# Kernel tuning notes

Hardware: AMD Instinct MI355X
Metric: run time of the kernel (lower is better)

The kernel has to match this reference:

```python
import jax, jax.numpy as jnp
import numpy as np

RES = (32, 32, 32)   # S, H, W
WS = 4               # window size (cubic)
SHIFT = 2            # shift size
NH = 6               # num heads
C = 192              # dim
EPS = 1e-5


def _rel_pos_index(ws):
    coords = np.stack(np.meshgrid(np.arange(ws), np.arange(ws), np.arange(ws), indexing='ij'))
    cf = coords.reshape(3, -1)                      # (3, N)
    rc = (cf[:, :, None] - cf[:, None, :]).transpose(1, 2, 0).astype(np.int64)  # (N,N,3)
    rc[..., 0] += ws - 1
    rc[..., 1] += ws - 1
    rc[..., 2] += ws - 1
    rc[..., 0] *= 3 * ws - 1
    rc[..., 1] *= 2 * ws - 1
    return rc.sum(-1)                               # (N, N)

_RPI = jnp.asarray(_rel_pos_index(WS))


def _ln(x, g, b):
    m = jnp.mean(x, axis=-1, keepdims=True)
    v = jnp.mean(jnp.square(x - m), axis=-1, keepdims=True)
    return (x - m) * jax.lax.rsqrt(v + EPS) * g + b


def setup_inputs():
    key = jax.random.key(0)
    ks = jax.random.split(key, 12)
    B, L = 2, RES[0] * RES[1] * RES[2]
    nW, N = 512, WS ** 3
    Hd = 4 * C
    p = lambda k, s: jax.random.normal(k, s, jnp.float32) * 0.02
    return {
        'x': jax.random.normal(ks[0], (B, L, C), jnp.float32),
        'mask_matrix': jax.random.normal(ks[1], (nW, N, N), jnp.float32),
        'skip': jax.random.normal(ks[2], (B, L, C), jnp.float32),
        'x_up': jax.random.normal(ks[3], (B, L, C), jnp.float32),
        'norm1_g': jnp.ones((C,), jnp.float32), 'norm1_b': jnp.zeros((C,), jnp.float32),
        'kv_w': p(ks[4], (C, 2 * C)), 'kv_b': jnp.zeros((2 * C,), jnp.float32),
        'rpb_table': p(ks[5], ((2 * WS - 1) ** 3, NH)),
        'proj_w': p(ks[6], (C, C)), 'proj_b': jnp.zeros((C,), jnp.float32),
        'norm2_g': jnp.ones((C,), jnp.float32), 'norm2_b': jnp.zeros((C,), jnp.float32),
        'fc1_w': p(ks[7], (C, Hd)), 'fc1_b': jnp.zeros((Hd,), jnp.float32),
        'fc2_w': p(ks[8], (Hd, C)), 'fc2_b': jnp.zeros((C,), jnp.float32),
    }


def reference(x, mask_matrix, skip, x_up, norm1_g, norm1_b, kv_w, kv_b, rpb_table,
              proj_w, proj_b, norm2_g, norm2_b, fc1_w, fc1_b, fc2_w, fc2_b):
    B, L, _ = x.shape
    S, H, W = RES
    ws, N = WS, WS ** 3
    hd = C // NH
    scale = hd ** -0.5

    sn = _ln(skip, norm1_g, norm1_b).reshape(B, S, H, W, C)
    qn = _ln(x_up, norm1_g, norm1_b).reshape(B, S, H, W, C)
    # cyclic shift (shift_size > 0)
    sn = jnp.roll(sn, (-SHIFT, -SHIFT, -SHIFT), axis=(1, 2, 3))
    qn = jnp.roll(qn, (-SHIFT, -SHIFT, -SHIFT), axis=(1, 2, 3))

    def part(t):  # window partition -> (B*nW, N, C)
        t = t.reshape(B, S // ws, ws, H // ws, ws, W // ws, ws, C)
        return t.transpose(0, 1, 3, 5, 2, 4, 6, 7).reshape(-1, N, C)

    skw, qw = part(sn), part(qn)
    B_ = skw.shape[0]

    kv = (skw @ kv_w + kv_b).reshape(B_, N, 2, NH, hd)
    k = kv[:, :, 0].transpose(0, 2, 1, 3)   # (B_, NH, N, hd)
    v = kv[:, :, 1].transpose(0, 2, 1, 3)
    q = qw.reshape(B_, N, NH, hd).transpose(0, 2, 1, 3) * scale

    attn = jnp.einsum('bhqd,bhkd->bhqk', q, k)
    rpb = rpb_table[_RPI.reshape(-1)].reshape(N, N, NH).transpose(2, 0, 1)  # (NH, N, N)
    attn = attn + rpb[None]
    nW = mask_matrix.shape[0]
    attn = attn.reshape(B, nW, NH, N, N) + mask_matrix[None, :, None]
    attn = jax.nn.softmax(attn.reshape(B_, NH, N, N), axis=-1)

    out = jnp.einsum('bhqk,bhkd->bhqd', attn, v).transpose(0, 2, 1, 3).reshape(B_, N, C)
    out = out @ proj_w + proj_b

    # window reverse
    out = out.reshape(B, S // ws, H // ws, W // ws, ws, ws, ws, C)
    out = out.transpose(0, 1, 4, 2, 5, 3, 6, 7).reshape(B, S, H, W, C)
    out = jnp.roll(out, (SHIFT, SHIFT, SHIFT), axis=(1, 2, 3)).reshape(B, L, C)

    x = x + out
    h = _ln(x, norm2_g, norm2_b)
    h = jax.nn.gelu(h @ fc1_w + fc1_b, approximate=False) @ fc2_w + fc2_b
    return x + h
```

## Files before the change

kernel.cpp:

```cpp
#include <hip/hip_runtime.h>
#include <math.h>

typedef unsigned short u16;
typedef __bf16 bf16x8 __attribute__((ext_vector_type(8)));
typedef float f32x4 __attribute__((ext_vector_type(4)));
typedef unsigned short u16x8 __attribute__((ext_vector_type(8)));

#define SHIFT 2

static __device__ __forceinline__ f32x4 mfma16(bf16x8 a, bf16x8 b, f32x4 c) {
  return __builtin_amdgcn_mfma_f32_16x16x32_bf16(a, b, c, 0, 0, 0);
}
static __device__ __forceinline__ u16 f2bf(float f) {
  unsigned u = __builtin_bit_cast(unsigned, f);
  unsigned r = u + 0x7fffu + ((u >> 16) & 1u);
  return (u16)(r >> 16);
}
static __device__ __forceinline__ float bf2f(u16 u) {
  unsigned v = (unsigned)u << 16;
  return __builtin_bit_cast(float, v);
}
static __device__ __forceinline__ void stage16(const u16* g, u16* lbase, int lane) {
#if __has_builtin(__builtin_amdgcn_global_load_lds)
  __builtin_amdgcn_global_load_lds(
      (const __attribute__((address_space(1))) unsigned int*)g,
      (__attribute__((address_space(3))) unsigned int*)lbase, 16, 0, 0);
#else
  *(u16x8*)(lbase + lane * 8) = *(const u16x8*)g;
#endif
}

#define OFF_KVWT  ((size_t)0)
#define OFF_PRWT  (OFF_KVWT + 384*192*2)
#define OFF_FC1WT (OFF_PRWT + 192*192*2)
#define OFF_FC2WT (OFF_FC1WT + 768*192*2)
#define OFF_SKW   (OFF_FC2WT + 192*768*2)
#define OFF_QW    (OFF_SKW + (size_t)65536*192*2)
#define OFF_KVB   (OFF_QW + (size_t)65536*192*2)
#define OFF_HN    (OFF_KVB + (size_t)65536*384*2)
#define OFF_PO    (OFF_HN + (size_t)65536*192*2)

__global__ __launch_bounds__(256) void k_prep(
    const float* __restrict__ kv_w, const float* __restrict__ proj_w,
    const float* __restrict__ fc1_w, const float* __restrict__ fc2_w,
    u16* __restrict__ kvT, u16* __restrict__ prT,
    u16* __restrict__ f1T, u16* __restrict__ f2T) {
  int i = blockIdx.x * 256 + threadIdx.x;
  if (i < 192 * 384) kvT[(i % 384) * 192 + i / 384] = f2bf(kv_w[i]);
  if (i < 192 * 192) prT[(i % 192) * 192 + i / 192] = f2bf(proj_w[i]);
  if (i < 192 * 768) f1T[(i % 768) * 192 + i / 768] = f2bf(fc1_w[i]);
  if (i < 768 * 192) f2T[(i % 192) * 768 + i / 192] = f2bf(fc2_w[i]);
}

__global__ __launch_bounds__(256) void k_ln_part(
    const float* __restrict__ skip, const float* __restrict__ x_up,
    const float* __restrict__ gam, const float* __restrict__ bet,
    u16* __restrict__ skw, u16* __restrict__ qw) {
  int row = blockIdx.x * 4 + (threadIdx.x >> 6);
  int lane = threadIdx.x & 63;
  const float* sp = skip + (size_t)row * 192;
  const float* qp = x_up + (size_t)row * 192;
  float sv[3], qv[3], ss = 0.f, qs = 0.f;
#pragma unroll
  for (int j = 0; j < 3; j++) {
    sv[j] = sp[lane + 64 * j]; qv[j] = qp[lane + 64 * j];
    ss += sv[j]; qs += qv[j];
  }
#pragma unroll
  for (int m = 1; m < 64; m <<= 1) { ss += __shfl_xor(ss, m, 64); qs += __shfl_xor(qs, m, 64); }
  float sm = ss * (1.f / 192.f), qm = qs * (1.f / 192.f);
  float s2 = 0.f, q2 = 0.f;
#pragma unroll
  for (int j = 0; j < 3; j++) { float d = sv[j] - sm; s2 += d * d; d = qv[j] - qm; q2 += d * d; }
#pragma unroll
  for (int m = 1; m < 64; m <<= 1) { s2 += __shfl_xor(s2, m, 64); q2 += __shfl_xor(q2, m, 64); }
  float sr = rsqrtf(s2 * (1.f / 192.f) + 1e-5f), qr = rsqrtf(q2 * (1.f / 192.f) + 1e-5f);
  int b = row >> 15, l = row & 32767;
  int s = l >> 10, h = (l >> 5) & 31, w = l & 31;
  int s_ = (s - SHIFT) & 31, h_ = (h - SHIFT) & 31, w_ = (w - SHIFT) & 31;
  int wIdx = ((s_ >> 2) * 8 + (h_ >> 2)) * 8 + (w_ >> 2);
  int n = ((s_ & 3) * 4 + (h_ & 3)) * 4 + (w_ & 3);
  size_t orow = ((size_t)(b * 512 + wIdx) * 64 + n) * 192;
  const float scale = 0.17677669529663687f;
#pragma unroll
  for (int j = 0; j < 3; j++) {
    int cc = lane + 64 * j;
    float gg = gam[cc], bb = bet[cc];
    skw[orow + cc] = f2bf((sv[j] - sm) * sr * gg + bb);
    qw[orow + cc]  = f2bf(((qv[j] - qm) * qr * gg + bb) * scale);
  }
}

__global__ __launch_bounds__(256, 2) void k_kv(
    const u16* __restrict__ A, const u16* __restrict__ BT,
    const float* __restrict__ bias, u16* __restrict__ outh) {
  __shared__ u16 lw[192 * 192];
  int mb = blockIdx.x, nb = blockIdx.y;
  int tid = threadIdx.x, l = tid & 63, wv = tid >> 6, g = l >> 4, c = l & 15;
  int wr = wv >> 1, wc = wv & 1;
#pragma unroll
  for (int i = 0; i < 18; i++) {
    int CI = i * 256 + tid;
    int row = CI / 24, ch = CI % 24;
    int sch = (ch & 24) | ((ch ^ row) & 7);
    stage16(BT + (size_t)(nb * 192 + row) * 192 + sch * 8, lw + (i * 256 + wv * 64) * 8, l);
  }
  __syncthreads();
  f32x4 acc[4][6] = {};
#pragma unroll
  for (int ks = 0; ks < 6; ks++) {
    bf16x8 a[4];
#pragma unroll
    for (int m = 0; m < 4; m++)
      a[m] = *(const bf16x8*)&A[(size_t)(mb * 128 + wr * 64 + m * 16 + c) * 192 + ks * 32 + g * 8];
#pragma unroll
    for (int n = 0; n < 6; n++) {
      int col = wc * 96 + n * 16 + c;
      int ch = ks * 4 + g;
      int chp = (ch & 24) | ((ch ^ col) & 7);
      bf16x8 b = *(const bf16x8*)&lw[col * 192 + chp * 8];
#pragma unroll
      for (int m = 0; m < 4; m++) acc[m][n] = mfma16(a[m], b, acc[m][n]);
    }
  }
#pragma unroll
  for (int n = 0; n < 6; n++)
#pragma unroll
    for (int m = 0; m < 4; m++) {
      int col = nb * 192 + wc * 96 + n * 16 + c;
      float bb = bias[col];
#pragma unroll
      for (int r = 0; r < 4; r++) {
        int row = mb * 128 + wr * 64 + m * 16 + g * 4 + r;
        outh[(size_t)row * 384 + col] = f2bf(acc[m][n][r] + bb);
      }
    }
}

__global__ __launch_bounds__(384, 4) void k_attn_mega(
    const u16* __restrict__ qw, const u16* __restrict__ kvb,
    const float* __restrict__ rpb, const float* __restrict__ mask,
    const u16* __restrict__ prT, const float* __restrict__ proj_b,
    const float* __restrict__ x, const float* __restrict__ g2,
    const float* __restrict__ b2, u16* __restrict__ hn, u16* __restrict__ po) {
  __shared__ __align__(16) char smem[25600 + 13824 + 17408 + 8256];
  u16* lv = (u16*)smem;
  u16* lo = (u16*)smem;
  u16* lp = (u16*)(smem + 25600);
  float* pf = (float*)(smem + 25600);
  float* lmaskf = (float*)(smem + 25600 + 13824);
  float* lrpbf  = (float*)(smem + 25600 + 13824 + 17408);
  int b_ = blockIdx.x, wIdx = b_ & 511;
  int tid = threadIdx.x, l = tid & 63, wv = tid >> 6, g = l >> 4, c = l & 15;
  int h = wv;
#pragma unroll
  for (int i = 0; i < 4; i++) {
    int CI = i * 384 + tid;
    int row = CI / 24, ch = CI % 24;
    stage16(kvb + ((size_t)b_ * 64 + row) * 384 + 192 + ch * 8,
            lv + (i * 384 + wv * 64) * 8, l);
  }
  bf16x8 qa[4], kb[4];
#pragma unroll
  for (int m = 0; m < 4; m++)
    qa[m] = *(const bf16x8*)&qw[((size_t)b_ * 64 + m * 16 + c) * 192 + h * 32 + g * 8];
#pragma unroll
  for (int n = 0; n < 4; n++)
    kb[n] = *(const bf16x8*)&kvb[((size_t)b_ * 64 + n * 16 + c) * 384 + h * 32 + g * 8];
  const float* mrow = mask + (size_t)wIdx * 4096;
#pragma unroll
  for (int i = 0; i < 3; i++) {
    int idx = i * 384 + tid;
    if (idx < 1024) {
      float4 mv = *(const float4*)&mrow[idx * 4];
      int row = idx >> 4, c4 = idx & 15;
      *(float4*)&lmaskf[row * 68 + c4 * 4] = mv;
    }
  }
#pragma unroll
  for (int i = 0; i < 6; i++) {
    int idx = i * 384 + tid;
    if (idx < 2058) lrpbf[idx] = rpb[idx];
  }
  __syncthreads();
  bf16x8 vb[2][2];
#pragma unroll
  for (int kk = 0; kk < 2; kk++)
#pragma unroll
    for (int nd = 0; nd < 2; nd++) {
      union { u16 u[8]; bf16x8 v; } bb;
#pragma unroll
      for (int j = 0; j < 8; j++)
        bb.u[j] = lv[(kk * 32 + g * 8 + j) * 192 + h * 32 + nd * 16 + c];
      vb[kk][nd] = bb.v;
    }
  __syncthreads();
  f32x4 acc[4][4] = {};
#pragma unroll
  for (int m = 0; m < 4; m++)
#pragma unroll
    for (int n = 0; n < 4; n++) acc[m][n] = mfma16(qa[m], kb[n], acc[m][n]);
  f32x4 oacc[4][2] = {};
#pragma unroll
  for (int m = 0; m < 4; m++) {
#pragma unroll
    for (int r = 0; r < 4; r++) {
      int qr = m * 16 + g * 4 + r;
      int qs = qr >> 4, qh = (qr >> 2) & 3, qx = qr & 3;
      float vals[4];
#pragma unroll
      for (int n = 0; n < 4; n++) {
        int kc = n * 16 + c;
        int ks = kc >> 4, kh = (kc >> 2) & 3, kx = kc & 3;
        int idx = (qs - ks + 3) * 11 + (qh - kh + 3) * 7 + (qx - kx + 3);
        vals[n] = acc[m][n][r] + lrpbf[idx * 6 + h] + lmaskf[qr * 68 + kc];
      }
      float mx = fmaxf(fmaxf(vals[0], vals[1]), fmaxf(vals[2], vals[3]));
#pragma unroll
      for (int mm = 1; mm < 16; mm <<= 1) mx = fmaxf(mx, __shfl_xor(mx, mm, 64));
      float sum = 0.f;
#pragma unroll
      for (int n = 0; n < 4; n++) { vals[n] = __expf(vals[n] - mx); sum += vals[n]; }
#pragma unroll
      for (int mm = 1; mm < 16; mm <<= 1) sum += __shfl_xor(sum, mm, 64);
      float inv = 1.f / sum;
#pragma unroll
      for (int n = 0; n < 4; n++)
        lp[h * 1152 + (g * 4 + r) * 72 + n * 16 + c] = f2bf(vals[n] * inv);
    }
#pragma unroll
    for (int kk = 0; kk < 2; kk++) {
      bf16x8 pa = *(const bf16x8*)&lp[h * 1152 + c * 72 + kk * 32 + g * 8];
#pragma unroll
      for (int nd = 0; nd < 2; nd++) oacc[m][nd] = mfma16(pa, vb[kk][nd], oacc[m][nd]);
    }
  }
#pragma unroll
  for (int m = 0; m < 4; m++)
#pragma unroll
    for (int nd = 0; nd < 2; nd++)
#pragma unroll
      for (int r = 0; r < 4; r++)
        lo[(m * 16 + g * 4 + r) * 200 + h * 32 + nd * 16 + c] = f2bf(oacc[m][nd][r]);
  __syncthreads();
  f32x4 pacc[4][2] = {};
#pragma unroll
  for (int ks = 0; ks < 6; ks++) {
    bf16x8 pa[4];
#pragma unroll
    for (int m = 0; m < 4; m++)
      pa[m] = *(const bf16x8*)&lo[(m * 16 + c) * 200 + ks * 32 + g * 8];
#pragma unroll
    for (int n = 0; n < 2; n++) {
      bf16x8 pb = *(const bf16x8*)&prT[(size_t)(wv * 32 + n * 16 + c) * 192 + ks * 32 + g * 8];
#pragma unroll
      for (int m = 0; m < 4; m++) pacc[m][n] = mfma16(pa[m], pb, pacc[m][n]);
    }
  }
  int bI = b_ >> 9;
  int wS = wIdx >> 6, wH = (wIdx >> 3) & 7, wW = wIdx & 7;
  float yv[4][2][4];
#pragma unroll
  for (int m = 0; m < 4; m++)
#pragma unroll
    for (int r = 0; r < 4; r++) {
      int tok = m * 16 + g * 4 + r;
      int inS = tok >> 4, inH = (tok >> 2) & 3, inW = tok & 3;
      int s = (wS * 4 + inS + SHIFT) & 31;
      int hh = (wH * 4 + inH + SHIFT) & 31;
      int ww = (wW * 4 + inW + SHIFT) & 31;
      size_t base = ((size_t)bI * 32768 + ((size_t)s * 32 + hh) * 32 + ww) * 192;
      float sum = 0.f, sq = 0.f;
#pragma unroll
      for (int n = 0; n < 2; n++) {
        int col = wv * 32 + n * 16 + c;
        float v = pacc[m][n][r] + proj_b[col];
        po[base + col] = f2bf(v);
        float y = v + x[base + col];
        yv[m][n][r] = y;
        sum += y; sq += y * y;
      }
#pragma unroll
      for (int mm = 1; mm < 16; mm <<= 1) { sum += __shfl_xor(sum, mm, 64); sq += __shfl_xor(sq, mm, 64); }
      if (c == 0) { pf[tok * 16 + wv] = sum; pf[tok * 16 + 8 + wv] = sq; }
    }
  __syncthreads();
#pragma unroll
  for (int m = 0; m < 4; m++)
#pragma unroll
    for (int r = 0; r < 4; r++) {
      int tok = m * 16 + g * 4 + r;
      int inS = tok >> 4, inH = (tok >> 2) & 3, inW = tok & 3;
      int s = (wS * 4 + inS + SHIFT) & 31;
      int hh = (wH * 4 + inH + SHIFT) & 31;
      int ww = (wW * 4 + inW + SHIFT) & 31;
      size_t base = ((size_t)bI * 32768 + ((size_t)s * 32 + hh) * 32 + ww) * 192;
      float su = 0.f, qu = 0.f;
#pragma unroll
      for (int w6 = 0; w6 < 6; w6++) { su += pf[tok * 16 + w6]; qu += pf[tok * 16 + 8 + w6]; }
      float mu = su * (1.f / 192.f);
      float rs = rsqrtf(qu * (1.f / 192.f) - mu * mu + 1e-5f);
#pragma unroll
      for (int n = 0; n < 2; n++) {
        int col = wv * 32 + n * 16 + c;
        hn[base + col] = f2bf((yv[m][n][r] - mu) * rs * g2[col] + b2[col]);
      }
    }
}

__global__ __launch_bounds__(256, 2) void k_mlp(
    const u16* __restrict__ hn, const u16* __restrict__ f1T,
    const u16* __restrict__ f2T, const float* __restrict__ b1,
    const float* __restrict__ b2f, const float* __restrict__ x,
    const u16* __restrict__ po, float* __restrict__ out) {
  __shared__ u16 lds[29184];
  u16* f1c = lds;
  u16* f2c = lds + 12288;
  u16* h1c = lds + 24576;
  int tid = threadIdx.x, l = tid & 63, wv = tid >> 6, g = l >> 4, c = l & 15;
  size_t tokbase = (size_t)blockIdx.x * 64;
#pragma unroll
  for (int i = 0; i < 6; i++) {
    int CI = i * 256 + wv * 64 + l;
    int row = CI / 24, chp = CI % 24;
    int sch = (chp & 24) | ((chp ^ row) & 7);
    stage16(hn + (tokbase + row) * 192 + sch * 8, f1c + (i * 256 + wv * 64) * 8, l);
  }
  __syncthreads();
  bf16x8 hb[4][6];
#pragma unroll
  for (int tf = 0; tf < 4; tf++)
#pragma unroll
    for (int ks = 0; ks < 6; ks++) {
      int ch = ks * 4 + g;
      int chp = (ch & 24) | ((ch ^ c) & 7);
      hb[tf][ks] = *(const bf16x8*)&f1c[(tf * 16 + c) * 192 + chp * 8];
    }
  f32x4 acc2[3][4] = {};
#pragma unroll 1
  for (int ko = 0; ko < 12; ko++) {
    __syncthreads();
#pragma unroll
    for (int i = 0; i < 6; i++) {
      int CI = i * 256 + wv * 64 + l;
      int row = CI / 24, chp = CI % 24;
      int sch = (chp & 24) | ((chp ^ row) & 7);
      stage16(f1T + (size_t)(ko * 64 + row) * 192 + sch * 8,
              f1c + (i * 256 + wv * 64) * 8, l);
    }
#pragma unroll
    for (int i = 0; i < 6; i++) {
      int CI = i * 256 + wv * 64 + l;
      int row = CI >> 3, chp = CI & 7;
      int sch = chp ^ (row & 7);
      stage16(f2T + (size_t)row * 768 + ko * 64 + sch * 8,
              f2c + (i * 256 + wv * 64) * 8, l);
    }
    __syncthreads();
    f32x4 acc1[4] = {};
#pragma unroll
    for (int ks = 0; ks < 6; ks++) {
      int ch = ks * 4 + g;
      int chp = (ch & 24) | ((ch ^ c) & 7);
      bf16x8 wa = *(const bf16x8*)&f1c[(wv * 16 + c) * 192 + chp * 8];
#pragma unroll
      for (int tf = 0; tf < 4; tf++) acc1[tf] = mfma16(wa, hb[tf][ks], acc1[tf]);
    }
    float4 b1v = *(const float4*)&b1[ko * 64 + wv * 16 + g * 4];
#pragma unroll
    for (int tf = 0; tf < 4; tf++) {
      unsigned pk[2];
#pragma unroll
      for (int p = 0; p < 2; p++) {
        unsigned lohi[2];
#pragma unroll
        for (int q = 0; q < 2; q++) {
          int r = p * 2 + q;
          float v = acc1[tf][r] + (r == 0 ? b1v.x : r == 1 ? b1v.y : r == 2 ? b1v.z : b1v.w);
          float u2 = v * (1.5957691216f + 0.0713548163f * v * v);
          v = v * (1.f / (1.f + __expf(-u2)));
          lohi[q] = f2bf(v);
        }
        pk[p] = lohi[0] | (lohi[1] << 16);
      }
      *(uint2*)&h1c[(tf * 16 + c) * 72 + wv * 16 + g * 4] = make_uint2(pk[0], pk[1]);
    }
    __syncthreads();
#pragma unroll
    for (int ck = 0; ck < 2; ck++) {
      bf16x8 a2[4];
#pragma unroll
      for (int tf = 0; tf < 4; tf++)
        a2[tf] = *(const bf16x8*)&h1c[(tf * 16 + c) * 72 + ck * 32 + g * 8];
#pragma unroll
      for (int of = 0; of < 3; of++) {
        int ch = ck * 4 + g;
        int chp = ch ^ (c & 7);
        bf16x8 wb = *(const bf16x8*)&f2c[(wv * 48 + of * 16 + c) * 64 + chp * 8];
#pragma unroll
        for (int tf = 0; tf < 4; tf++) acc2[of][tf] = mfma16(a2[tf], wb, acc2[of][tf]);
      }
    }
  }
#pragma unroll
  for (int of = 0; of < 3; of++)
#pragma unroll
    for (int tf = 0; tf < 4; tf++) {
      int col = wv * 48 + of * 16 + c;
      float bb = b2f[col];
#pragma unroll
      for (int r = 0; r < 4; r++) {
        size_t tok = tokbase + tf * 16 + g * 4 + r;
        size_t base = tok * 192 + col;
        out[base] = acc2[of][tf][r] + bb + x[base] + bf2f(po[base]);
      }
    }
}

extern "C" void kernel_launch(void* const* d_in, const int* in_sizes, int n_in,
                              void* d_out, int out_size, void* d_ws, size_t ws_size,
                              hipStream_t stream) {
  const float* x      = (const float*)d_in[0];
  const float* mask   = (const float*)d_in[1];
  const float* skip   = (const float*)d_in[2];
  const float* x_up   = (const float*)d_in[3];
  const float* n1g    = (const float*)d_in[4];
  const float* n1b    = (const float*)d_in[5];
  const float* kv_w   = (const float*)d_in[6];
  const float* kv_b   = (const float*)d_in[7];
  const float* rpb    = (const float*)d_in[8];
  const float* proj_w = (const float*)d_in[9];
  const float* proj_b = (const float*)d_in[10];
  const float* n2g    = (const float*)d_in[11];
  const float* n2b    = (const float*)d_in[12];
  const float* fc1_w  = (const float*)d_in[13];
  const float* fc1_b  = (const float*)d_in[14];
  const float* fc2_w  = (const float*)d_in[15];
  const float* fc2_b  = (const float*)d_in[16];
  char* ws = (char*)d_ws;
  u16* kvT  = (u16*)(ws + OFF_KVWT);
  u16* prT  = (u16*)(ws + OFF_PRWT);
  u16* f1T  = (u16*)(ws + OFF_FC1WT);
  u16* f2T  = (u16*)(ws + OFF_FC2WT);
  u16* skw  = (u16*)(ws + OFF_SKW);
  u16* qw   = (u16*)(ws + OFF_QW);
  u16* kvb  = (u16*)(ws + OFF_KVB);
  u16* hn   = (u16*)(ws + OFF_HN);
  u16* po   = (u16*)(ws + OFF_PO);
  float* out = (float*)d_out;

  k_prep<<<dim3(576), dim3(256), 0, stream>>>(kv_w, proj_w, fc1_w, fc2_w, kvT, prT, f1T, f2T);
  k_ln_part<<<dim3(16384), dim3(256), 0, stream>>>(skip, x_up, n1g, n1b, skw, qw);
  k_kv<<<dim3(512, 2), dim3(256), 0, stream>>>(skw, kvT, kv_b, kvb);
  k_attn_mega<<<dim3(1024), dim3(384), 0, stream>>>(
      qw, kvb, rpb, mask, prT, proj_b, x, n2g, n2b, hn, po);
  k_mlp<<<dim3(1024), dim3(256), 0, stream>>>(hn, f1T, f2T, fc1_b, fc2_b, x, po, out);
}
```

Before: 260.8 us.

## Precompute expanded bf16 relative-position bias and read mask directly from global

The relative position bias is expanded once per call in the prep kernel into a per-head 64x64 bf16 table, and the mask is no longer staged in LDS; both are read directly from global memory inside the softmax loop. This cuts the attention kernel's shared memory from about 65 KB to 38 KB and raises the launch-bounds occupancy hint from 4 to 6 blocks. It adds a sync before the output LDS reuse, since the P buffer now overlaps the output staging area. The costs are strided, uncoalesced global loads for mask and bias in the hot loop, and the bias rounded to bf16.

```diff
diff --git a/kernel.cpp b/kernel.cpp
--- a/kernel.cpp
+++ b/kernel.cpp
@@ -39,17 +39,26 @@
 #define OFF_KVB   (OFF_QW + (size_t)65536*192*2)
 #define OFF_HN    (OFF_KVB + (size_t)65536*384*2)
 #define OFF_PO    (OFF_HN + (size_t)65536*192*2)
+#define OFF_RPBG  (OFF_PO + (size_t)65536*192*2)
 
 __global__ __launch_bounds__(256) void k_prep(
     const float* __restrict__ kv_w, const float* __restrict__ proj_w,
     const float* __restrict__ fc1_w, const float* __restrict__ fc2_w,
+    const float* __restrict__ rpb,
     u16* __restrict__ kvT, u16* __restrict__ prT,
-    u16* __restrict__ f1T, u16* __restrict__ f2T) {
+    u16* __restrict__ f1T, u16* __restrict__ f2T, u16* __restrict__ rpbg) {
   int i = blockIdx.x * 256 + threadIdx.x;
   if (i < 192 * 384) kvT[(i % 384) * 192 + i / 384] = f2bf(kv_w[i]);
   if (i < 192 * 192) prT[(i % 192) * 192 + i / 192] = f2bf(proj_w[i]);
   if (i < 192 * 768) f1T[(i % 768) * 192 + i / 768] = f2bf(fc1_w[i]);
   if (i < 768 * 192) f2T[(i % 192) * 768 + i / 192] = f2bf(fc2_w[i]);
+  if (i < 24576) {
+    int h = i >> 12, rem = i & 4095, qr = rem >> 6, kc = rem & 63;
+    int qs = qr >> 4, qh = (qr >> 2) & 3, qx = qr & 3;
+    int ks = kc >> 4, kh = (kc >> 2) & 3, kx = kc & 3;
+    int idx = (qs - ks + 3) * 11 + (qh - kh + 3) * 7 + (qx - kx + 3);
+    rpbg[i] = f2bf(rpb[idx * 6 + h]);
+  }
 }
 
 __global__ __launch_bounds__(256) void k_ln_part(
@@ -137,19 +146,17 @@
     }
 }
 
-__global__ __launch_bounds__(384, 4) void k_attn_mega(
+__global__ __launch_bounds__(384, 6) void k_attn_mega(
     const u16* __restrict__ qw, const u16* __restrict__ kvb,
-    const float* __restrict__ rpb, const float* __restrict__ mask,
+    const u16* __restrict__ rpbg, const float* __restrict__ mask,
     const u16* __restrict__ prT, const float* __restrict__ proj_b,
     const float* __restrict__ x, const float* __restrict__ g2,
     const float* __restrict__ b2, u16* __restrict__ hn, u16* __restrict__ po) {
-  __shared__ __align__(16) char smem[25600 + 13824 + 17408 + 8256];
+  __shared__ __align__(16) char smem[38400];
   u16* lv = (u16*)smem;
   u16* lo = (u16*)smem;
-  u16* lp = (u16*)(smem + 25600);
+  u16* lp = (u16*)(smem + 24576);
   float* pf = (float*)(smem + 25600);
-  float* lmaskf = (float*)(smem + 25600 + 13824);
-  float* lrpbf  = (float*)(smem + 25600 + 13824 + 17408);
   int b_ = blockIdx.x, wIdx = b_ & 511;
   int tid = threadIdx.x, l = tid & 63, wv = tid >> 6, g = l >> 4, c = l & 15;
   int h = wv;
@@ -167,21 +174,6 @@
 #pragma unroll
   for (int n = 0; n < 4; n++)
     kb[n] = *(const bf16x8*)&kvb[((size_t)b_ * 64 + n * 16 + c) * 384 + h * 32 + g * 8];
-  const float* mrow = mask + (size_t)wIdx * 4096;
-#pragma unroll
-  for (int i = 0; i < 3; i++) {
-    int idx = i * 384 + tid;
-    if (idx < 1024) {
-      float4 mv = *(const float4*)&mrow[idx * 4];
-      int row = idx >> 4, c4 = idx & 15;
-      *(float4*)&lmaskf[row * 68 + c4 * 4] = mv;
-    }
-  }
-#pragma unroll
-  for (int i = 0; i < 6; i++) {
-    int idx = i * 384 + tid;
-    if (idx < 2058) lrpbf[idx] = rpb[idx];
-  }
   __syncthreads();
   bf16x8 vb[2][2];
 #pragma unroll
@@ -200,20 +192,19 @@
   for (int m = 0; m < 4; m++)
 #pragma unroll
     for (int n = 0; n < 4; n++) acc[m][n] = mfma16(qa[m], kb[n], acc[m][n]);
+  const float* mrow = mask + (size_t)wIdx * 4096;
+  const u16* rg = rpbg + h * 4096;
   f32x4 oacc[4][2] = {};
 #pragma unroll
   for (int m = 0; m < 4; m++) {
 #pragma unroll
     for (int r = 0; r < 4; r++) {
       int qr = m * 16 + g * 4 + r;
-      int qs = qr >> 4, qh = (qr >> 2) & 3, qx = qr & 3;
       float vals[4];
 #pragma unroll
       for (int n = 0; n < 4; n++) {
         int kc = n * 16 + c;
-        int ks = kc >> 4, kh = (kc >> 2) & 3, kx = kc & 3;
-        int idx = (qs - ks + 3) * 11 + (qh - kh + 3) * 7 + (qx - kx + 3);
-        vals[n] = acc[m][n][r] + lrpbf[idx * 6 + h] + lmaskf[qr * 68 + kc];
+        vals[n] = acc[m][n][r] + bf2f(rg[qr * 64 + kc]) + mrow[qr * 64 + kc];
       }
       float mx = fmaxf(fmaxf(vals[0], vals[1]), fmaxf(vals[2], vals[3]));
 #pragma unroll
@@ -235,6 +226,7 @@
       for (int nd = 0; nd < 2; nd++) oacc[m][nd] = mfma16(pa, vb[kk][nd], oacc[m][nd]);
     }
   }
+  __syncthreads();
 #pragma unroll
   for (int m = 0; m < 4; m++)
 #pragma unroll
@@ -447,12 +439,14 @@
   u16* kvb  = (u16*)(ws + OFF_KVB);
   u16* hn   = (u16*)(ws + OFF_HN);
   u16* po   = (u16*)(ws + OFF_PO);
+  u16* rpbg = (u16*)(ws + OFF_RPBG);
   float* out = (float*)d_out;
 
-  k_prep<<<dim3(576), dim3(256), 0, stream>>>(kv_w, proj_w, fc1_w, fc2_w, kvT, prT, f1T, f2T);
+  k_prep<<<dim3(576), dim3(256), 0, stream>>>(kv_w, proj_w, fc1_w, fc2_w, rpb,
+                                              kvT, prT, f1T, f2T, rpbg);
   k_ln_part<<<dim3(16384), dim3(256), 0, stream>>>(skip, x_up, n1g, n1b, skw, qw);
   k_kv<<<dim3(512, 2), dim3(256), 0, stream>>>(skw, kvT, kv_b, kvb);
   k_attn_mega<<<dim3(1024), dim3(384), 0, stream>>>(
-      qw, kvb, rpb, mask, prT, proj_b, x, n2g, n2b, hn, po);
+      qw, kvb, rpbg, mask, prT, proj_b, x, n2g, n2b, hn, po);
   k_mlp<<<dim3(1024), dim3(256), 0, stream>>>(hn, f1T, f2T, fc1_b, fc2_b, x, po, out);
 }
```

Measured after the change: 316.0 us. 1.21x slower.
